# Kernel tuning notes

Measured on AMD Instinct MI355X. Metric: run time of the kernel, lower is better.

The kernel has to match this reference:

```python
import jax, jax.numpy as jnp
import numpy as np

HEADS = 8
DIM_HEAD = 64
DIM = 512
B, N = 4, 2048
SCALE = DIM_HEAD ** -0.5


def setup_inputs() -> dict:
    key = jax.random.key(0)
    k1, k2, k3, k4, k5, k6 = jax.random.split(key, 6)
    inner = HEADS * DIM_HEAD
    s = DIM ** -0.5
    return {
        "input_feature": jax.random.normal(k1, (B, N, DIM), dtype=jnp.float32),
        "mask": jax.random.randint(k2, (B, N), 0, 2, dtype=jnp.int32),
        "Wq": jax.random.normal(k3, (inner, DIM), dtype=jnp.float32) * s,
        "Wk": jax.random.normal(k4, (inner, DIM), dtype=jnp.float32) * s,
        "Wv": jax.random.normal(k5, (inner, DIM), dtype=jnp.float32) * s,
        "Wout": jax.random.normal(k6, (DIM, inner), dtype=jnp.float32) * s,
    }


def reference(input_feature, mask, Wq, Wk, Wv, Wout):
    # Conv1d with kernel_size=1, no bias == per-token linear: out = W @ x_channels
    q = jnp.einsum('bnc,dc->bnd', input_feature, Wq)  # [B, N, H*Dh]
    k = jnp.einsum('bnc,dc->bnd', input_feature, Wk)
    v = jnp.einsum('bnc,dc->bnd', input_feature, Wv)

    # '(n c)' channel layout is head-major -> reshape to [B, N, H, Dh], move head out front
    def split_heads(t):
        return t.reshape(B, N, HEADS, DIM_HEAD).transpose(2, 0, 1, 3)  # [H, B, N, Dh]

    q, k, v = split_heads(q), split_heads(k), split_heads(v)

    scores = jnp.einsum('hbtd,hbsd->hbts', q, k) * SCALE  # [H, B, N, N]
    # masked_fill(mask == 0, 1e-9): fill with small CONSTANT (not -inf), faithful to source
    m = (mask == 0)[None, :, None, :]  # [1, B, 1, N]
    scores = jnp.where(m, jnp.float32(1e-9), scores)
    att = jax.nn.softmax(scores, axis=-1)
    out = jnp.einsum('hbts,hbsd->hbtd', att, v)  # [H, B, N, Dh]

    # '(n b) tokens c -> b (n c) tokens' : head-major channel concat
    out = out.transpose(1, 2, 0, 3).reshape(B, N, HEADS * DIM_HEAD)  # [B, N, H*Dh]
    out = jnp.einsum('bnd,ed->bne', out, Wout)  # [B, N, DIM]
    return out
```

## Files before the change

### kernel.cpp

```cpp
#include <hip/hip_runtime.h>
#include <hip/hip_bf16.h>

typedef __attribute__((ext_vector_type(8))) short short8;
typedef __attribute__((ext_vector_type(4))) short short4_t;
typedef __attribute__((ext_vector_type(4))) float float4_;

#define LOG2E 1.4426950408889634f

__device__ __forceinline__ short f2bf(float f) {
    unsigned int u = __builtin_bit_cast(unsigned int, f);
    u = (u + 0x7FFFu + ((u >> 16) & 1u)) >> 16;
    return (short)u;
}

__device__ __forceinline__ unsigned pk2bf(float a, float b) {
    unsigned ua = __builtin_bit_cast(unsigned, a) + 0x8000u;
    unsigned ub = __builtin_bit_cast(unsigned, b) + 0x8000u;
    return __builtin_amdgcn_perm(ub, ua, 0x07060302);
}

__device__ __forceinline__ void pl32swap(unsigned &a, unsigned &b) {
    auto r = __builtin_amdgcn_permlane32_swap(a, b, false, false);
    a = r[0]; b = r[1];
}
__device__ __forceinline__ void pl16swap(unsigned &a, unsigned &b) {
    auto r = __builtin_amdgcn_permlane16_swap(a, b, false, false);
    a = r[0]; b = r[1];
}

union U4 { unsigned u[4]; short8 s; };

__device__ __forceinline__ void gload_lds16(const short* g, short* l) {
    __builtin_amdgcn_global_load_lds((const __attribute__((address_space(1))) void*)g,
                                     (__attribute__((address_space(3))) void*)l, 16, 0, 0);
}

__global__ __launch_bounds__(256) void cvt_kernel(
    const float* __restrict__ X, const float* __restrict__ Wq, const float* __restrict__ Wk,
    const float* __restrict__ Wv, const float* __restrict__ Wo,
    short* __restrict__ Xb, short* __restrict__ Wqkvb, short* __restrict__ Wob) {
    int i = blockIdx.x * 256 + threadIdx.x;
    const float* src; short* dst; float sc = 1.0f;
    if (i < 1048576) { src = X + (size_t)i * 4; dst = Xb + (size_t)i * 4; }
    else {
        int w = i - 1048576; int sec = w >> 16; int j = (w & 65535) * 4;
        if (sec == 0)      { src = Wq + j; dst = Wqkvb + j; sc = 0.125f * LOG2E; }
        else if (sec == 1) { src = Wk + j; dst = Wqkvb + 262144 + j; }
        else if (sec == 2) { src = Wv + j; dst = Wqkvb + 524288 + j; }
        else               { src = Wo + j; dst = Wob + j; }
    }
    float4 v = *(const float4*)src;
    short4_t o;
    o[0] = f2bf(v.x * sc); o[1] = f2bf(v.y * sc); o[2] = f2bf(v.z * sc); o[3] = f2bf(v.w * sc);
    *(short4_t*)dst = o;
}

__global__ __launch_bounds__(256) void gemm_qkv(const short* __restrict__ A, const short* __restrict__ B,
                                                const int* __restrict__ mask,
                                                short* __restrict__ Qb, short* __restrict__ Kb,
                                                short* __restrict__ Vtb) {
    __shared__ __align__(16) short smemAB[2 * 8192];
    __shared__ int maskL[128];
    short* At = smemAB;
    short* Bt = smemAB + 8192;
    constexpr int K = 512;
    int tid = threadIdx.x;
    int wid = tid >> 6, lane = tid & 63;
    int quad = lane >> 4, cc = lane & 15;
    int c7 = cc & 7;
    int wr = wid >> 1, wc = wid & 1;
    int m0 = blockIdx.y * 128, n0 = blockIdx.x * 128;
    if (tid < 128) maskL[tid] = mask[m0 + tid];

    const short* gA[4]; const short* gB[4]; int lofs[4];
#pragma unroll
    for (int p = 0; p < 4; ++p) {
        int slot = p * 256 + tid;
        int r = slot >> 3, c = slot & 7;
        int cs = (c ^ (r & 7)) * 8;
        gA[p] = A + (size_t)(m0 + r) * K + cs;
        gB[p] = B + (size_t)(n0 + r) * K + cs;
        lofs[p] = slot * 8;
    }
    short8 arg[4], brg[4];
#pragma unroll
    for (int p = 0; p < 4; ++p) { arg[p] = *(const short8*)gA[p]; brg[p] = *(const short8*)gB[p]; }

    float4_ acc[4][4] = {};

    for (int kk = 0; kk < K; kk += 64) {
        __syncthreads();
#pragma unroll
        for (int p = 0; p < 4; ++p) {
            *(short8*)(At + lofs[p]) = arg[p];
            *(short8*)(Bt + lofs[p]) = brg[p];
        }
        if (kk < K - 64) {
#pragma unroll
            for (int p = 0; p < 4; ++p) {
                arg[p] = *(const short8*)(gA[p] + kk + 64);
                brg[p] = *(const short8*)(gB[p] + kk + 64);
            }
        }
        __syncthreads();
#pragma unroll
        for (int kc = 0; kc < 2; ++kc) {
            short8 af[4], bf[4];
#pragma unroll
            for (int i = 0; i < 4; ++i)
                af[i] = *(const short8*)(At + (wr * 64 + i * 16 + cc) * 64 + (((kc * 4 + quad) ^ c7) * 8));
#pragma unroll
            for (int j = 0; j < 4; ++j)
                bf[j] = *(const short8*)(Bt + (wc * 64 + j * 16 + cc) * 64 + (((kc * 4 + quad) ^ c7) * 8));
#pragma unroll
            for (int i = 0; i < 4; ++i)
#pragma unroll
                for (int j = 0; j < 4; ++j)
                    acc[i][j] = __builtin_amdgcn_mfma_f32_16x16x32_bf16(af[i], bf[j], acc[i][j], 0, 0, 0);
        }
    }

    int which = n0 >> 9;
    int b = m0 >> 11;
    if (which == 2) {
        __syncthreads();
        short* T = smemAB;
#pragma unroll
        for (int i = 0; i < 4; ++i) {
#pragma unroll
            for (int j = 0; j < 4; ++j) {
                int d_l = wc * 64 + j * 16 + cc;
                int nnb = wr * 64 + i * 16 + quad * 4;
                int G = nnb >> 3, half = (nnb >> 2) & 1;
                int Gs = G ^ (d_l & 15);
                short4_t pv;
                pv[0] = f2bf(acc[i][j][0]); pv[1] = f2bf(acc[i][j][1]);
                pv[2] = f2bf(acc[i][j][2]); pv[3] = f2bf(acc[i][j][3]);
                *(short4_t*)(T + d_l * 128 + Gs * 8 + half * 4) = pv;
            }
        }
        __syncthreads();
#pragma unroll
        for (int p = 0; p < 8; ++p) {
            int slot = p * 256 + tid;
            int d = slot >> 4, G = slot & 15;
            short8 v = *(const short8*)(T + d * 128 + ((G ^ (d & 15)) * 8));
            *(short8*)(Vtb + ((size_t)(b * 512 + (n0 & 511) + d)) * 2048 + (m0 & 2047) + G * 8) = v;
        }
    } else {
        short* dst = which ? Kb : Qb;
#pragma unroll
        for (int i = 0; i < 4; ++i) {
#pragma unroll
            for (int j = 0; j < 4; ++j) {
#pragma unroll
                for (int r = 0; r < 4; ++r) {
                    int lm = wr * 64 + i * 16 + quad * 4 + r;
                    int nn = (m0 & 2047) + lm;
                    int hd = (n0 & 511) + wc * 64 + j * 16 + cc;
                    int h = hd >> 6, dh = hd & 63;
                    float v = acc[i][j][r];
                    if (which == 1 && maskL[lm] == 0) v = 0.0f;
                    dst[((((size_t)b * 8 + h) * 2048 + nn) * 64) + dh] = f2bf(v);
                }
            }
        }
    }
}

__global__ __launch_bounds__(256, 2) void attn_kernel(const short* __restrict__ Q, const short* __restrict__ Kg,
                                                      const short* __restrict__ Vt,
                                                      short* __restrict__ AO) {
    __shared__ __align__(16) short KbufL[2 * 4096];

    int tid = threadIdx.x;
    int w = tid >> 6, lane = tid & 63;
    int quad = lane >> 4, cc = lane & 15;
    int c7 = cc & 7;
    int bh = blockIdx.x, b = bh >> 3, h = bh & 7;
    int t0 = blockIdx.y * 128 + w * 32;
    size_t kbase = (size_t)bh * 2048 * 64;
    size_t vbase = (size_t)b * 512 * 2048 + (size_t)h * 64 * 2048;

    short8 qf[2][2];
#pragma unroll
    for (int tb = 0; tb < 2; ++tb)
#pragma unroll
        for (int kc = 0; kc < 2; ++kc)
            qf[tb][kc] = *(const short8*)(Q + kbase + (size_t)(t0 + tb * 16 + cc) * 64 + kc * 32 + quad * 8);

    int koff[4][2];
#pragma unroll
    for (int sb = 0; sb < 4; ++sb)
#pragma unroll
        for (int kc = 0; kc < 2; ++kc)
            koff[sb][kc] = (sb * 16 + cc) * 64 + (((kc * 4 + quad) ^ c7) * 8);

    int sA = tid >> 3, cA = tid & 7;
    const short* gK0 = Kg + kbase + (size_t)sA * 64 + ((cA ^ (sA & 7)) * 8);
    const short* gK1 = gK0 + 32 * 64;
    int ld0 = tid * 8, ld1 = tid * 8 + 2048;
    short8 krg0 = *(const short8*)gK0, krg1 = *(const short8*)gK1;
    gK0 += 4096; gK1 += 4096;
    *(short8*)(KbufL + ld0) = krg0; *(short8*)(KbufL + ld1) = krg1;
    krg0 = *(const short8*)gK0; krg1 = *(const short8*)gK1;
    gK0 += 4096; gK1 += 4096;

    const short* gVb = Vt + vbase + (size_t)cc * 2048 + quad * 8;
    short8 vfA[4][2], vfB[4][2];
#pragma unroll
    for (int db = 0; db < 4; ++db)
#pragma unroll
        for (int kc = 0; kc < 2; ++kc)
            vfA[db][kc] = *(const short8*)(gVb + db * 32768 + kc * 32);

    float4_ o[2][4] = {};
    float lp[2] = {0.f, 0.f};

    auto body = [&](short8 (&vfc)[4][2], short8 (&vfn)[4][2], int it) {
        __syncthreads();
        int cur = it & 1;
        const short* Kt = KbufL + cur * 4096;
        if (it < 31) {
            short* Kn = KbufL + (cur ^ 1) * 4096;
            *(short8*)(Kn + ld0) = krg0;
            *(short8*)(Kn + ld1) = krg1;
        }
        if (it < 30) {
            krg0 = *(const short8*)gK0; krg1 = *(const short8*)gK1;
            gK0 += 4096; gK1 += 4096;
        }
        if (it < 31) {
            int s1 = (it + 1) * 64;
#pragma unroll
            for (int db = 0; db < 4; ++db)
#pragma unroll
                for (int kc = 0; kc < 2; ++kc)
                    vfn[db][kc] = *(const short8*)(gVb + db * 32768 + kc * 32 + s1);
        }

        float4_ acc[4][2];
        __builtin_amdgcn_s_setprio(1);
#pragma unroll
        for (int sb = 0; sb < 4; ++sb) {
            short8 kf0 = *(const short8*)(Kt + koff[sb][0]);
            short8 kf1 = *(const short8*)(Kt + koff[sb][1]);
#pragma unroll
            for (int tb = 0; tb < 2; ++tb) {
                float4_ z = {0.f, 0.f, 0.f, 0.f};
                z = __builtin_amdgcn_mfma_f32_16x16x32_bf16(kf0, qf[tb][0], z, 0, 0, 0);
                acc[sb][tb] = __builtin_amdgcn_mfma_f32_16x16x32_bf16(kf1, qf[tb][1], z, 0, 0, 0);
            }
        }
        __builtin_amdgcn_s_setprio(0);

        unsigned Wp[4][2][2];
#pragma unroll
        for (int sb = 0; sb < 4; ++sb)
#pragma unroll
            for (int tb = 0; tb < 2; ++tb) {
                float x0 = __builtin_amdgcn_exp2f(acc[sb][tb][0]);
                float x1 = __builtin_amdgcn_exp2f(acc[sb][tb][1]);
                float x2 = __builtin_amdgcn_exp2f(acc[sb][tb][2]);
                float x3 = __builtin_amdgcn_exp2f(acc[sb][tb][3]);
                lp[tb] += (x0 + x1) + (x2 + x3);
                Wp[sb][tb][0] = pk2bf(x0, x1);
                Wp[sb][tb][1] = pk2bf(x2, x3);
            }

        short8 pa[2][2];
#pragma unroll
        for (int kc = 0; kc < 2; ++kc)
#pragma unroll
            for (int tb = 0; tb < 2; ++tb) {
                unsigned a0 = Wp[2 * kc][tb][0], a1 = Wp[2 * kc][tb][1];
                unsigned b0 = Wp[2 * kc + 1][tb][0], b1 = Wp[2 * kc + 1][tb][1];
                pl32swap(a0, b0); pl32swap(a1, b1);
                pl16swap(a0, b0); pl16swap(a1, b1);
                U4 u; u.u[0] = a0; u.u[1] = a1; u.u[2] = b0; u.u[3] = b1;
                pa[tb][kc] = u.s;
            }

        __builtin_amdgcn_s_setprio(1);
#pragma unroll
        for (int db = 0; db < 4; ++db)
#pragma unroll
            for (int tb = 0; tb < 2; ++tb) {
                o[tb][db] = __builtin_amdgcn_mfma_f32_16x16x32_bf16(pa[tb][0], vfc[db][0], o[tb][db], 0, 0, 0);
                o[tb][db] = __builtin_amdgcn_mfma_f32_16x16x32_bf16(pa[tb][1], vfc[db][1], o[tb][db], 0, 0, 0);
            }
        __builtin_amdgcn_s_setprio(0);
    };

#pragma unroll 1
    for (int it = 0; it < 32; it += 2) {
        body(vfA, vfB, it);
        body(vfB, vfA, it + 1);
    }

    float inv[2];
#pragma unroll
    for (int tb = 0; tb < 2; ++tb) {
        float s = lp[tb];
        s += __shfl_xor(s, 16, 64);
        s += __shfl_xor(s, 32, 64);
        inv[tb] = 1.0f / s;
    }
#pragma unroll
    for (int tb = 0; tb < 2; ++tb)
#pragma unroll
        for (int r = 0; r < 4; ++r) {
            int tl = tb * 16 + quad * 4 + r;
            float iv = __shfl(inv[tb], quad * 4 + r, 64);
            size_t rowbase = ((size_t)(b * 2048 + t0 + tl)) * 512 + h * 64;
#pragma unroll
            for (int db = 0; db < 4; ++db)
                AO[rowbase + db * 16 + cc] = f2bf(o[tb][db][r] * iv);
        }
}

__global__ __launch_bounds__(256) void gemm_out(const short* __restrict__ A, const short* __restrict__ B,
                                                float* __restrict__ C) {
    __shared__ short At[64 * 64];
    __shared__ short Bt[64 * 64];
    constexpr int K = 512;
    int tid = threadIdx.x;
    int wid = tid >> 6, lane = tid & 63;
    int quad = lane >> 4, cc = lane & 15;
    int c7 = cc & 7;
    int wr = wid >> 1, wc = wid & 1;
    int m0 = blockIdx.y * 64, n0 = blockIdx.x * 64;

    float4_ acc[2][2] = {};

    for (int kk = 0; kk < K; kk += 64) {
#pragma unroll
        for (int p = 0; p < 2; ++p) {
            int slot = p * 256 + tid;
            int r = slot >> 3, c = slot & 7;
            int cs = (c ^ (r & 7)) * 8;
            gload_lds16(A + (size_t)(m0 + r) * K + kk + cs, At + slot * 8);
            gload_lds16(B + (size_t)(n0 + r) * K + kk + cs, Bt + slot * 8);
        }
        __syncthreads();
#pragma unroll
        for (int kc = 0; kc < 2; ++kc) {
            short8 af[2], bf[2];
#pragma unroll
            for (int i = 0; i < 2; ++i)
                af[i] = *(const short8*)(At + (wr * 32 + i * 16 + cc) * 64 + (((kc * 4 + quad) ^ c7) * 8));
#pragma unroll
            for (int j = 0; j < 2; ++j)
                bf[j] = *(const short8*)(Bt + (wc * 32 + j * 16 + cc) * 64 + (((kc * 4 + quad) ^ c7) * 8));
#pragma unroll
            for (int i = 0; i < 2; ++i)
#pragma unroll
                for (int j = 0; j < 2; ++j)
                    acc[i][j] = __builtin_amdgcn_mfma_f32_16x16x32_bf16(af[i], bf[j], acc[i][j], 0, 0, 0);
        }
        __syncthreads();
    }

#pragma unroll
    for (int i = 0; i < 2; ++i)
#pragma unroll
        for (int j = 0; j < 2; ++j)
#pragma unroll
            for (int r = 0; r < 4; ++r) {
                int gm = m0 + wr * 32 + i * 16 + quad * 4 + r;
                int gn = n0 + wc * 32 + j * 16 + cc;
                C[(size_t)gm * 512 + gn] = acc[i][j][r];
            }
}

extern "C" void kernel_launch(void* const* d_in, const int* in_sizes, int n_in,
                              void* d_out, int out_size, void* d_ws, size_t ws_size,
                              hipStream_t stream) {
    const float* X  = (const float*)d_in[0];
    const int* mask = (const int*)d_in[1];
    const float* Wq = (const float*)d_in[2];
    const float* Wk = (const float*)d_in[3];
    const float* Wv = (const float*)d_in[4];
    const float* Wo = (const float*)d_in[5];

    char* ws = (char*)d_ws;
    short* Xbf   = (short*)(ws + 0);
    short* Wqkvb = (short*)(ws + 8388608);
    short* Wob   = (short*)(ws + 9961472);
    short* Qb    = (short*)(ws + 10485760);
    short* Kb    = (short*)(ws + 18874368);
    short* Vtb   = (short*)(ws + 27262976);
    short* AOb   = (short*)(ws + 35651584);

    cvt_kernel<<<5120, 256, 0, stream>>>(X, Wq, Wk, Wv, Wo, Xbf, Wqkvb, Wob);
    gemm_qkv<<<dim3(12, 64), 256, 0, stream>>>(Xbf, Wqkvb, mask, Qb, Kb, Vtb);
    attn_kernel<<<dim3(32, 16), 256, 0, stream>>>(Qb, Kb, Vtb, AOb);
    gemm_out<<<dim3(8, 128), 256, 0, stream>>>(AOb, Wob, (float*)d_out);
}
```

Before: 182.8 us.

## Stage V through shared memory and halve attention query tile per block

```diff
diff --git a/kernel.cpp b/kernel.cpp
--- a/kernel.cpp
+++ b/kernel.cpp
@@ -168,155 +168,129 @@
     }
 }
 
-__global__ __launch_bounds__(256, 2) void attn_kernel(const short* __restrict__ Q, const short* __restrict__ Kg,
+__global__ __launch_bounds__(256, 4) void attn_kernel(const short* __restrict__ Q, const short* __restrict__ Kg,
                                                       const short* __restrict__ Vt,
                                                       short* __restrict__ AO) {
     __shared__ __align__(16) short KbufL[2 * 4096];
+    __shared__ __align__(16) short VbufL[2 * 4096];
 
     int tid = threadIdx.x;
     int w = tid >> 6, lane = tid & 63;
     int quad = lane >> 4, cc = lane & 15;
     int c7 = cc & 7;
     int bh = blockIdx.x, b = bh >> 3, h = bh & 7;
-    int t0 = blockIdx.y * 128 + w * 32;
+    int t0 = blockIdx.y * 64 + w * 16;
     size_t kbase = (size_t)bh * 2048 * 64;
     size_t vbase = (size_t)b * 512 * 2048 + (size_t)h * 64 * 2048;
 
-    short8 qf[2][2];
-#pragma unroll
-    for (int tb = 0; tb < 2; ++tb)
+    short8 qf[2];
+#pragma unroll
+    for (int kc = 0; kc < 2; ++kc)
+        qf[kc] = *(const short8*)(Q + kbase + (size_t)(t0 + cc) * 64 + kc * 32 + quad * 8);
+
+    int koff[4][2];
+#pragma unroll
+    for (int rb = 0; rb < 4; ++rb)
 #pragma unroll
         for (int kc = 0; kc < 2; ++kc)
-            qf[tb][kc] = *(const short8*)(Q + kbase + (size_t)(t0 + tb * 16 + cc) * 64 + kc * 32 + quad * 8);
-
-    int koff[4][2];
-#pragma unroll
-    for (int sb = 0; sb < 4; ++sb)
-#pragma unroll
-        for (int kc = 0; kc < 2; ++kc)
-            koff[sb][kc] = (sb * 16 + cc) * 64 + (((kc * 4 + quad) ^ c7) * 8);
+            koff[rb][kc] = (rb * 16 + cc) * 64 + (((kc * 4 + quad) ^ c7) * 8);
 
     int sA = tid >> 3, cA = tid & 7;
     const short* gK0 = Kg + kbase + (size_t)sA * 64 + ((cA ^ (sA & 7)) * 8);
     const short* gK1 = gK0 + 32 * 64;
+    const short* gV0 = Vt + vbase + (size_t)sA * 2048 + ((cA ^ (sA & 7)) * 8);
+    const short* gV1 = gV0 + 32 * 2048;
     int ld0 = tid * 8, ld1 = tid * 8 + 2048;
+
     short8 krg0 = *(const short8*)gK0, krg1 = *(const short8*)gK1;
-    gK0 += 4096; gK1 += 4096;
+    short8 vrg0 = *(const short8*)gV0, vrg1 = *(const short8*)gV1;
+    gK0 += 4096; gK1 += 4096; gV0 += 64; gV1 += 64;
     *(short8*)(KbufL + ld0) = krg0; *(short8*)(KbufL + ld1) = krg1;
+    *(short8*)(VbufL + ld0) = vrg0; *(short8*)(VbufL + ld1) = vrg1;
     krg0 = *(const short8*)gK0; krg1 = *(const short8*)gK1;
-    gK0 += 4096; gK1 += 4096;
-
-    const short* gVb = Vt + vbase + (size_t)cc * 2048 + quad * 8;
-    short8 vfA[4][2], vfB[4][2];
-#pragma unroll
-    for (int db = 0; db < 4; ++db)
-#pragma unroll
-        for (int kc = 0; kc < 2; ++kc)
-            vfA[db][kc] = *(const short8*)(gVb + db * 32768 + kc * 32);
-
-    float4_ o[2][4] = {};
-    float lp[2] = {0.f, 0.f};
-
-    auto body = [&](short8 (&vfc)[4][2], short8 (&vfn)[4][2], int it) {
+    vrg0 = *(const short8*)gV0; vrg1 = *(const short8*)gV1;
+    gK0 += 4096; gK1 += 4096; gV0 += 64; gV1 += 64;
+
+    float4_ o[4] = {};
+    float lp = 0.f;
+
+#pragma unroll 2
+    for (int it = 0; it < 32; ++it) {
         __syncthreads();
         int cur = it & 1;
-        const short* Kt = KbufL + cur * 4096;
+        const short* Kt  = KbufL + cur * 4096;
+        const short* Vtt = VbufL + cur * 4096;
         if (it < 31) {
             short* Kn = KbufL + (cur ^ 1) * 4096;
-            *(short8*)(Kn + ld0) = krg0;
-            *(short8*)(Kn + ld1) = krg1;
+            short* Vn = VbufL + (cur ^ 1) * 4096;
+            *(short8*)(Kn + ld0) = krg0; *(short8*)(Kn + ld1) = krg1;
+            *(short8*)(Vn + ld0) = vrg0; *(short8*)(Vn + ld1) = vrg1;
         }
         if (it < 30) {
             krg0 = *(const short8*)gK0; krg1 = *(const short8*)gK1;
-            gK0 += 4096; gK1 += 4096;
-        }
-        if (it < 31) {
-            int s1 = (it + 1) * 64;
-#pragma unroll
-            for (int db = 0; db < 4; ++db)
-#pragma unroll
-                for (int kc = 0; kc < 2; ++kc)
-                    vfn[db][kc] = *(const short8*)(gVb + db * 32768 + kc * 32 + s1);
-        }
-
-        float4_ acc[4][2];
+            vrg0 = *(const short8*)gV0; vrg1 = *(const short8*)gV1;
+            gK0 += 4096; gK1 += 4096; gV0 += 64; gV1 += 64;
+        }
+
+        float4_ acc[4];
         __builtin_amdgcn_s_setprio(1);
 #pragma unroll
         for (int sb = 0; sb < 4; ++sb) {
             short8 kf0 = *(const short8*)(Kt + koff[sb][0]);
             short8 kf1 = *(const short8*)(Kt + koff[sb][1]);
-#pragma unroll
-            for (int tb = 0; tb < 2; ++tb) {
-                float4_ z = {0.f, 0.f, 0.f, 0.f};
-                z = __builtin_amdgcn_mfma_f32_16x16x32_bf16(kf0, qf[tb][0], z, 0, 0, 0);
-                acc[sb][tb] = __builtin_amdgcn_mfma_f32_16x16x32_bf16(kf1, qf[tb][1], z, 0, 0, 0);
-            }
+            float4_ z = {0.f, 0.f, 0.f, 0.f};
+            z = __builtin_amdgcn_mfma_f32_16x16x32_bf16(kf0, qf[0], z, 0, 0, 0);
+            acc[sb] = __builtin_amdgcn_mfma_f32_16x16x32_bf16(kf1, qf[1], z, 0, 0, 0);
         }
         __builtin_amdgcn_s_setprio(0);
 
-        unsigned Wp[4][2][2];
-#pragma unroll
-        for (int sb = 0; sb < 4; ++sb)
-#pragma unroll
-            for (int tb = 0; tb < 2; ++tb) {
-                float x0 = __builtin_amdgcn_exp2f(acc[sb][tb][0]);
-                float x1 = __builtin_amdgcn_exp2f(acc[sb][tb][1]);
-                float x2 = __builtin_amdgcn_exp2f(acc[sb][tb][2]);
-                float x3 = __builtin_amdgcn_exp2f(acc[sb][tb][3]);
-                lp[tb] += (x0 + x1) + (x2 + x3);
-                Wp[sb][tb][0] = pk2bf(x0, x1);
-                Wp[sb][tb][1] = pk2bf(x2, x3);
-            }
-
-        short8 pa[2][2];
-#pragma unroll
-        for (int kc = 0; kc < 2; ++kc)
-#pragma unroll
-            for (int tb = 0; tb < 2; ++tb) {
-                unsigned a0 = Wp[2 * kc][tb][0], a1 = Wp[2 * kc][tb][1];
-                unsigned b0 = Wp[2 * kc + 1][tb][0], b1 = Wp[2 * kc + 1][tb][1];
-                pl32swap(a0, b0); pl32swap(a1, b1);
-                pl16swap(a0, b0); pl16swap(a1, b1);
-                U4 u; u.u[0] = a0; u.u[1] = a1; u.u[2] = b0; u.u[3] = b1;
-                pa[tb][kc] = u.s;
-            }
+        unsigned Wp[4][2];
+#pragma unroll
+        for (int sb = 0; sb < 4; ++sb) {
+            float x0 = __builtin_amdgcn_exp2f(acc[sb][0]);
+            float x1 = __builtin_amdgcn_exp2f(acc[sb][1]);
+            float x2 = __builtin_amdgcn_exp2f(acc[sb][2]);
+            float x3 = __builtin_amdgcn_exp2f(acc[sb][3]);
+            lp += (x0 + x1) + (x2 + x3);
+            Wp[sb][0] = pk2bf(x0, x1);
+            Wp[sb][1] = pk2bf(x2, x3);
+        }
+
+        short8 pa[2];
+#pragma unroll
+        for (int kc = 0; kc < 2; ++kc) {
+            unsigned a0 = Wp[2 * kc][0], a1 = Wp[2 * kc][1];
+            unsigned b0 = Wp[2 * kc + 1][0], b1 = Wp[2 * kc + 1][1];
+            pl32swap(a0, b0); pl32swap(a1, b1);
+            pl16swap(a0, b0); pl16swap(a1, b1);
+            U4 u; u.u[0] = a0; u.u[1] = a1; u.u[2] = b0; u.u[3] = b1;
+            pa[kc] = u.s;
+        }
 
         __builtin_amdgcn_s_setprio(1);
 #pragma unroll
+        for (int db = 0; db < 4; ++db) {
+            short8 vf0 = *(const short8*)(Vtt + koff[db][0]);
+            short8 vf1 = *(const short8*)(Vtt + koff[db][1]);
+            o[db] = __builtin_amdgcn_mfma_f32_16x16x32_bf16(pa[0], vf0, o[db], 0, 0, 0);
+            o[db] = __builtin_amdgcn_mfma_f32_16x16x32_bf16(pa[1], vf1, o[db], 0, 0, 0);
+        }
+        __builtin_amdgcn_s_setprio(0);
+    }
+
+    float s = lp;
+    s += __shfl_xor(s, 16, 64);
+    s += __shfl_xor(s, 32, 64);
+    float inv = 1.0f / s;
+#pragma unroll
+    for (int r = 0; r < 4; ++r) {
+        int tl = quad * 4 + r;
+        float iv = __shfl(inv, tl, 64);
+        size_t rowbase = ((size_t)(b * 2048 + t0 + tl)) * 512 + h * 64;
+#pragma unroll
         for (int db = 0; db < 4; ++db)
-#pragma unroll
-            for (int tb = 0; tb < 2; ++tb) {
-                o[tb][db] = __builtin_amdgcn_mfma_f32_16x16x32_bf16(pa[tb][0], vfc[db][0], o[tb][db], 0, 0, 0);
-                o[tb][db] = __builtin_amdgcn_mfma_f32_16x16x32_bf16(pa[tb][1], vfc[db][1], o[tb][db], 0, 0, 0);
-            }
-        __builtin_amdgcn_s_setprio(0);
-    };
-
-#pragma unroll 1
-    for (int it = 0; it < 32; it += 2) {
-        body(vfA, vfB, it);
-        body(vfB, vfA, it + 1);
-    }
-
-    float inv[2];
-#pragma unroll
-    for (int tb = 0; tb < 2; ++tb) {
-        float s = lp[tb];
-        s += __shfl_xor(s, 16, 64);
-        s += __shfl_xor(s, 32, 64);
-        inv[tb] = 1.0f / s;
-    }
-#pragma unroll
-    for (int tb = 0; tb < 2; ++tb)
-#pragma unroll
-        for (int r = 0; r < 4; ++r) {
-            int tl = tb * 16 + quad * 4 + r;
-            float iv = __shfl(inv[tb], quad * 4 + r, 64);
-            size_t rowbase = ((size_t)(b * 2048 + t0 + tl)) * 512 + h * 64;
-#pragma unroll
-            for (int db = 0; db < 4; ++db)
-                AO[rowbase + db * 16 + cc] = f2bf(o[tb][db][r] * iv);
-        }
+            AO[rowbase + db * 16 + cc] = f2bf(o[db][r] * iv);
+    }
 }
 
 __global__ __launch_bounds__(256) void gemm_out(const short* __restrict__ A, const short* __restrict__ B,
@@ -394,6 +368,6 @@
 
     cvt_kernel<<<5120, 256, 0, stream>>>(X, Wq, Wk, Wv, Wo, Xbf, Wqkvb, Wob);
     gemm_qkv<<<dim3(12, 64), 256, 0, stream>>>(Xbf, Wqkvb, mask, Qb, Kb, Vtb);
-    attn_kernel<<<dim3(32, 16), 256, 0, stream>>>(Qb, Kb, Vtb, AOb);
+    attn_kernel<<<dim3(32, 32), 256, 0, stream>>>(Qb, Kb, Vtb, AOb);
     gemm_out<<<dim3(8, 128), 256, 0, stream>>>(AOb, Wob, (float*)d_out);
 }
```

Result: faster. 164.2 us (-10.2%).
